# Kernel tuning notes

Hardware: AMD Instinct MI355X
Metric: run time of the kernel (lower is better)

## Reference

```python
import math
import jax, jax.numpy as jnp
import numpy as np

B, T, DIM = 1, 2048, 2048
NH, NKV = 32, 8
HD = DIM // NH  # 64
REP = NH // NKV  # 4


def _rope(x):
    # x: [b, h, t, d]; rotates as in the torch module (half-split, concat form)
    d = x.shape[-1]
    half = d // 2
    t = x.shape[2]
    freqs = jnp.arange(half, dtype=x.dtype) / max(half, 1)
    angles = jnp.arange(t, dtype=x.dtype)[:, None] * freqs[None, :]  # [t, half]
    sin = jnp.sin(angles)[None, None]  # [1,1,t,half]
    cos = jnp.cos(angles)[None, None]
    x1, x2 = x[..., :half], x[..., half:]
    return jnp.concatenate([x1 * cos - x2 * sin, x1 * sin + x2 * cos], axis=-1)


def setup_inputs() -> dict:
    key = jax.random.key(0)
    k1, k2, k3 = jax.random.split(key, 3)
    sd = 1.0 / math.sqrt(DIM)
    return {
        "x": jax.random.normal(k1, (B, T, DIM), dtype=jnp.float32),
        "Wqkv": jax.random.normal(k2, ((NH + 2 * NKV) * HD, DIM), dtype=jnp.float32) * sd,
        "Wproj": jax.random.normal(k3, (DIM, DIM), dtype=jnp.float32) * sd,
        "q_gain": jnp.ones((NH,), dtype=jnp.float32),
        "attn_temp": jnp.ones((NH,), dtype=jnp.float32),
    }


def reference(x, Wqkv, Wproj, q_gain, attn_temp):
    b, t, c = x.shape
    qkv = x @ Wqkv.T  # [b, t, (NH+2*NKV)*HD]
    q, k, v = jnp.split(qkv, [NH * HD, (NH + NKV) * HD], axis=2)
    q = q.reshape(b, t, NH, HD).transpose(0, 2, 1, 3)   # [b, NH, t, HD]
    k = k.reshape(b, t, NKV, HD).transpose(0, 2, 1, 3)  # [b, NKV, t, HD]
    v = v.reshape(b, t, NKV, HD).transpose(0, 2, 1, 3)
    # GQA expand (repeat_interleave along head axis)
    k = jnp.repeat(k, REP, axis=1)  # [b, NH, t, HD]
    v = jnp.repeat(v, REP, axis=1)
    q = _rope(q)
    k = _rope(k)
    q = q * (q_gain * attn_temp)[None, :, None, None]
    scale = 1.0 / math.sqrt(HD)
    scores = jnp.einsum('bhqd,bhkd->bhqk', q, k) * scale
    causal = jnp.tril(jnp.ones((t, t), dtype=bool))
    scores = jnp.where(causal[None, None], scores, jnp.finfo(scores.dtype).min)
    attn = jax.nn.softmax(scores, axis=-1)
    y = jnp.einsum('bhqk,bhkd->bhqd', attn, v)  # [b, NH, t, HD]
    y = y.transpose(0, 2, 1, 3).reshape(b, t, c)
    return y @ Wproj.T
```

## Files before the change

### kernel.cpp

```cpp
#include <hip/hip_runtime.h>
#include <hip/hip_bf16.h>
#include <math.h>

typedef unsigned short u16;
typedef __attribute__((ext_vector_type(8))) short short8;
typedef __attribute__((ext_vector_type(4))) float f32x4;
typedef __attribute__((ext_vector_type(4))) unsigned short u16x4;
typedef __attribute__((ext_vector_type(4))) unsigned int u32x4;

#define DEVI static __device__ __forceinline__

DEVI u16 f2bf(float f){
  union { float f; unsigned u; } c; c.f = f;
  unsigned r = (c.u + 0x7fffu + ((c.u >> 16) & 1u)) >> 16;
  return (u16)r;
}

DEVI unsigned cvtpk(float lo, float hi){
  unsigned r;
  asm("v_cvt_pk_bf16_f32 %0, %1, %2" : "=v"(r) : "v"(lo), "v"(hi));
  return r;
}

DEVI void async16(const void* g, void* l){
  __builtin_amdgcn_global_load_lds(
    (const __attribute__((address_space(1))) unsigned int*)g,
    (__attribute__((address_space(3))) unsigned int*)l, 16, 0, 0);
}

#define WAIT_BAR(N) asm volatile("s_waitcnt vmcnt(" #N ") lgkmcnt(0)\n\ts_barrier" ::: "memory")

#define ACHUNK(r, g) (((r) << 2) | (((g) + ((r) >> 1)) & 3))
#define KCH(r, g) (((r) << 3) | (((g) + (r)) & 7))

__global__ __launch_bounds__(256) void cvt3(const float4* __restrict__ x,
                                            const float4* __restrict__ wq,
                                            const float4* __restrict__ wp,
                                            u16* __restrict__ xb,
                                            u16* __restrict__ wqb,
                                            u16* __restrict__ wpb){
  int i = blockIdx.x * 256 + threadIdx.x;
  const float4* s; u16* d; int off;
  if (i < 1048576)      { s = x;  d = xb;  off = i; }
  else if (i < 2621440) { s = wq; d = wqb; off = i - 1048576; }
  else                  { s = wp; d = wpb; off = i - 2621440; }
  float4 v = s[off];
  u16x4 o;
  o.x = f2bf(v.x); o.y = f2bf(v.y); o.z = f2bf(v.z); o.w = f2bf(v.w);
  *(u16x4*)(d + (size_t)off * 4) = o;
}

__global__ __launch_bounds__(256) void gemm_qkv(const u16* __restrict__ A,
                                                const u16* __restrict__ B,
                                                const float* __restrict__ qg,
                                                const float* __restrict__ at_,
                                                u16* __restrict__ qb,
                                                u16* __restrict__ kb,
                                                u16* __restrict__ vT){
  const int K = 2048;
  __shared__ __align__(16) u16 As[4][4096];
  __shared__ __align__(16) u16 Bs[4][4096];
  const int bid = blockIdx.x;
  const int xcd = bid & 7, pos = bid >> 3;
  const int xm = xcd & 1, xn = xcd >> 1;
  const int mIdx = xm * 8 + (pos & 7);
  const int nIdx = xn * 6 + (pos >> 3);
  const int tid  = threadIdx.x;
  const int lane = tid & 63, wid = tid >> 6;
  const int wr = wid >> 1, wc = wid & 1;
  const int fr = lane & 15, fg = lane >> 4;
  const int mBase = mIdx * 128, nBase = nIdx * 128;

  f32x4 acc[4][4];
  for (int m = 0; m < 4; ++m)
    for (int n = 0; n < 4; ++n)
      for (int e = 0; e < 4; ++e) acc[m][n][e] = 0.f;

  const int c0 = tid, c1 = tid + 256;
  const int p0 = c0 >> 2, q0 = ((c0 & 3) - (p0 >> 1)) & 3;
  const int p1 = c1 >> 2, q1 = ((c1 & 3) - (p1 >> 1)) & 3;
  const u16* Ab = A + (size_t)mBase * K;
  const u16* Bb = B + (size_t)nBase * K;

  int ca[4], cb[4];
#pragma unroll
  for (int m = 0; m < 4; ++m){ const int r = wr * 64 + m * 16 + fr; ca[m] = ACHUNK(r, fg); }
#pragma unroll
  for (int n = 0; n < 4; ++n){ const int r = wc * 64 + n * 16 + fr; cb[n] = ACHUNK(r, fg); }

#define STAGE_QKV(kt) do {                                                 \
    const int b_ = (kt) & 3;                                               \
    const int kO_ = (kt) * 32;                                             \
    async16(Ab + (size_t)p0 * K + kO_ + q0 * 8, As[b_] + c0 * 8);          \
    async16(Ab + (size_t)p1 * K + kO_ + q1 * 8, As[b_] + c1 * 8);          \
    async16(Bb + (size_t)p0 * K + kO_ + q0 * 8, Bs[b_] + c0 * 8);          \
    async16(Bb + (size_t)p1 * K + kO_ + q1 * 8, Bs[b_] + c1 * 8);          \
  } while (0)

  STAGE_QKV(0); STAGE_QKV(1); STAGE_QKV(2); STAGE_QKV(3);

#pragma unroll 1
  for (int p = 0; p < 32; ++p){
    if (p < 31) WAIT_BAR(8);
    else        WAIT_BAR(0);
#pragma unroll
    for (int kk = 0; kk < 2; ++kk){
      const int cur = (2 * p + kk) & 3;
      short8 a[4], b[4];
#pragma unroll
      for (int m = 0; m < 4; ++m)
        a[m] = *(const short8*)(As[cur] + ca[m] * 8);
#pragma unroll
      for (int n = 0; n < 4; ++n)
        b[n] = *(const short8*)(Bs[cur] + cb[n] * 8);
      __builtin_amdgcn_s_setprio(1);
#pragma unroll
      for (int m = 0; m < 4; ++m)
#pragma unroll
        for (int n = 0; n < 4; ++n)
          acc[m][n] = __builtin_amdgcn_mfma_f32_16x16x32_bf16(a[m], b[n], acc[m][n], 0, 0, 0);
      __builtin_amdgcn_s_setprio(0);
    }
    __builtin_amdgcn_s_barrier();
    if (p < 30){ STAGE_QKV(2 * p + 4); STAGE_QKV(2 * p + 5); }
  }
#undef STAGE_QKV

  const int nb64 = nIdx * 2 + wc;
  if (nb64 < 40){
    const bool isq = nb64 < 32;
    const int h = isq ? nb64 : (nb64 - 32);
    const float gsc = isq ? (qg[h] * at_[h] * 0.125f) : 1.0f;
    u16* dst = isq ? qb : kb;
#pragma unroll
    for (int m = 0; m < 4; ++m)
#pragma unroll
      for (int e = 0; e < 4; ++e){
        const int t = mBase + wr * 64 + m * 16 + fg * 4 + e;
        const float ft = (float)t;
#pragma unroll
        for (int np = 0; np < 2; ++np){
          const int d = np * 16 + fr;
          const float ang = ft * ((float)d * 0.03125f);
          float sn, cs; sincosf(ang, &sn, &cs);
          const float x1 = acc[m][np][e], x2 = acc[m][np + 2][e];
          u16* base = dst + ((size_t)h * 2048 + t) * 64 + d;
          base[0]  = f2bf((x1 * cs - x2 * sn) * gsc);
          base[32] = f2bf((x1 * sn + x2 * cs) * gsc);
        }
      }
  } else {
    const int h = nb64 - 40;
#pragma unroll
    for (int m = 0; m < 4; ++m){
      const int t0 = mBase + wr * 64 + m * 16 + fg * 4;
#pragma unroll
      for (int n = 0; n < 4; ++n){
        const int d = n * 16 + fr;
        u16x4 pk;
#pragma unroll
        for (int e = 0; e < 4; ++e) pk[e] = f2bf(acc[m][n][e]);
        *(u16x4*)(vT + ((size_t)h * 64 + d) * 2048 + t0) = pk;
      }
    }
  }
}

__global__ __launch_bounds__(256) void attn_fwd(const u16* __restrict__ qb,
                                                const u16* __restrict__ kb,
                                                const u16* __restrict__ vT,
                                                u16* __restrict__ yb){
  const int bx = blockIdx.x, h = blockIdx.y;
  const int hk = h >> 2;
  const int tid = threadIdx.x;
  const int lane = tid & 63, wid = tid >> 6;
  const int fr = lane & 15, fg = lane >> 4;

  __shared__ __align__(16) u16 Ks[2][4096];
  __shared__ __align__(16) u16 Vs[2][4096];

  const u16* kbh = kb + (size_t)hk * 2048 * 64;
  const u16* vTh = vT + (size_t)hk * 64 * 2048;

  const int c0 = tid, c1 = tid + 256;
  const int p0 = c0 >> 3, q0 = ((c0 & 7) - p0) & 7;
  const int p1 = c1 >> 3, q1 = ((c1 & 7) - p1) & 7;
  const int pr0 = ((p0 >> 5) << 5) | (((p0 >> 2) & 3) << 3) | (((p0 >> 4) & 1) << 2) | (p0 & 3);
  const int pr1 = ((p1 >> 5) << 5) | (((p1 >> 2) & 3) << 3) | (((p1 >> 4) & 1) << 2) | (p1 & 3);

  int ck[2][4];
#pragma unroll
  for (int kc = 0; kc < 2; ++kc)
#pragma unroll
    for (int cf = 0; cf < 4; ++cf)
      ck[kc][cf] = KCH(cf * 16 + fr, kc * 4 + fg);

#pragma unroll 1
  for (int seg = 0; seg < 2; ++seg){
    const int qt = seg ? (31 - bx) : bx;
    const int nt = qt + 1;
    const int qrow0 = qt * 64 + wid * 16;
    const int q = qrow0 + fr;

    short8 qf[2];
    {
      const u16* qp = qb + ((size_t)h * 2048 + q) * 64 + fg * 8;
      qf[0] = *(const short8*)(qp);
      qf[1] = *(const short8*)(qp + 32);
    }

    float mrow = -1e30f, lrow = 0.f;
    f32x4 o[4];
    for (int df = 0; df < 4; ++df)
      for (int e = 0; e < 4; ++e) o[df][e] = 0.f;

    async16(kbh + (size_t)pr0 * 64 + q0 * 8,  Ks[0] + (size_t)c0 * 8);
    async16(kbh + (size_t)pr1 * 64 + q1 * 8,  Ks[0] + (size_t)c1 * 8);
    async16(vTh + (size_t)p0 * 2048 + q0 * 8, Vs[0] + (size_t)c0 * 8);
    async16(vTh + (size_t)p1 * 2048 + q1 * 8, Vs[0] + (size_t)c1 * 8);

#pragma unroll 1
    for (int kt = 0; kt < nt; ++kt){
      const int cur = kt & 1;
      __syncthreads();
      if (kt + 1 < nt){
        const int nxt = cur ^ 1;
        const size_t kO = (size_t)(kt + 1) * 64;
        async16(kbh + (kO + pr0) * 64 + q0 * 8,        Ks[nxt] + (size_t)c0 * 8);
        async16(kbh + (kO + pr1) * 64 + q1 * 8,        Ks[nxt] + (size_t)c1 * 8);
        async16(vTh + (size_t)p0 * 2048 + kO + q0 * 8, Vs[nxt] + (size_t)c0 * 8);
        async16(vTh + (size_t)p1 * 2048 + kO + q1 * 8, Vs[nxt] + (size_t)c1 * 8);
      }
      const u16* Kb = Ks[cur];
      const u16* Vb = Vs[cur];

      f32x4 s[4];
      __builtin_amdgcn_s_setprio(1);
#pragma unroll
      for (int cf = 0; cf < 4; ++cf){
        for (int e = 0; e < 4; ++e) s[cf][e] = 0.f;
#pragma unroll
        for (int kc = 0; kc < 2; ++kc){
          short8 kf = *(const short8*)(Kb + ck[kc][cf] * 8);
          s[cf] = __builtin_amdgcn_mfma_f32_16x16x32_bf16(kf, qf[kc], s[cf], 0, 0, 0);
        }
      }
      __builtin_amdgcn_s_setprio(0);

      if (kt * 64 + 63 > qrow0){
#pragma unroll
        for (int cf = 0; cf < 4; ++cf){
          const int kb0 = kt * 64 + (cf >> 1) * 32 + (cf & 1) * 4 + fg * 8;
#pragma unroll
          for (int r = 0; r < 4; ++r)
            if (kb0 + r > q) s[cf][r] = -1e30f;
        }
      }

      float m0 = fmaxf(fmaxf(s[0][0], s[0][1]), fmaxf(s[0][2], s[0][3]));
      float m1 = fmaxf(fmaxf(s[1][0], s[1][1]), fmaxf(s[1][2], s[1][3]));
      float m2 = fmaxf(fmaxf(s[2][0], s[2][1]), fmaxf(s[2][2], s[2][3]));
      float m3 = fmaxf(fmaxf(s[3][0], s[3][1]), fmaxf(s[3][2], s[3][3]));
      float mt = fmaxf(fmaxf(m0, m1), fmaxf(m2, m3));
      mt = fmaxf(mt, __shfl_xor(mt, 16));
      mt = fmaxf(mt, __shfl_xor(mt, 32));
      if (!__all(mt <= mrow + 8.f)){
        const float mn = fmaxf(mrow, mt);
        const float al = __expf(mrow - mn);
        lrow *= al;
#pragma unroll
        for (int df = 0; df < 4; ++df)
#pragma unroll
          for (int e = 0; e < 4; ++e) o[df][e] *= al;
        mrow = mn;
      }
      float rs = 0.f;
#pragma unroll
      for (int cf = 0; cf < 4; ++cf){
#pragma unroll
        for (int r = 0; r < 4; ++r){
          s[cf][r] = __expf(s[cf][r] - mrow);
          rs += s[cf][r];
        }
      }
      rs += __shfl_xor(rs, 16);
      rs += __shfl_xor(rs, 32);
      lrow += rs;

      union { u32x4 u; short8 s8; } pb_0, pb_1;
      pb_0.u[0] = cvtpk(s[0][0], s[0][1]); pb_0.u[1] = cvtpk(s[0][2], s[0][3]);
      pb_0.u[2] = cvtpk(s[1][0], s[1][1]); pb_0.u[3] = cvtpk(s[1][2], s[1][3]);
      pb_1.u[0] = cvtpk(s[2][0], s[2][1]); pb_1.u[1] = cvtpk(s[2][2], s[2][3]);
      pb_1.u[2] = cvtpk(s[3][0], s[3][1]); pb_1.u[3] = cvtpk(s[3][2], s[3][3]);

      __builtin_amdgcn_s_setprio(1);
#pragma unroll
      for (int df = 0; df < 4; ++df){
        short8 v0 = *(const short8*)(Vb + ck[0][df] * 8);
        short8 v1 = *(const short8*)(Vb + ck[1][df] * 8);
        o[df] = __builtin_amdgcn_mfma_f32_16x16x32_bf16(v0, pb_0.s8, o[df], 0, 0, 0);
        o[df] = __builtin_amdgcn_mfma_f32_16x16x32_bf16(v1, pb_1.s8, o[df], 0, 0, 0);
      }
      __builtin_amdgcn_s_setprio(0);
    }
    __syncthreads();

    const float inv = 1.f / lrow;
#pragma unroll
    for (int df = 0; df < 4; ++df){
      u16x4 pk;
#pragma unroll
      for (int e = 0; e < 4; ++e) pk[e] = f2bf(o[df][e] * inv);
      *(u16x4*)(yb + (size_t)q * 2048 + h * 64 + df * 16 + fg * 4) = pk;
    }
  }
}

__global__ __launch_bounds__(256) void gemm_bt(const u16* __restrict__ A,
                                               const u16* __restrict__ B,
                                               float* __restrict__ C,
                                               int M, int N, int K){
  __shared__ __align__(16) u16 As[4][4096];
  __shared__ __align__(16) u16 Bs[4][4096];
  const int bid = blockIdx.x;
  const int xcd = bid & 7, pos = bid >> 3;
  const int xm = xcd & 1, xn = xcd >> 1;
  const int mIdx = xm * 8 + (pos & 7);
  const int nIdx = xn * 4 + (pos >> 3);
  const int tid  = threadIdx.x;
  const int lane = tid & 63, wid = tid >> 6;
  const int wr = wid >> 1, wc = wid & 1;
  const int fr = lane & 15, fg = lane >> 4;
  const int mBase = mIdx * 128, nBase = nIdx * 128;

  f32x4 acc[4][4];
  for (int m = 0; m < 4; ++m)
    for (int n = 0; n < 4; ++n)
      for (int e = 0; e < 4; ++e) acc[m][n][e] = 0.f;

  const int c0 = tid, c1 = tid + 256;
  const int p0 = c0 >> 2, q0 = ((c0 & 3) - (p0 >> 1)) & 3;
  const int p1 = c1 >> 2, q1 = ((c1 & 3) - (p1 >> 1)) & 3;
  const u16* Ab = A + (size_t)mBase * K;
  const u16* Bb = B + (size_t)nBase * K;

  int ca[4], cb[4];
#pragma unroll
  for (int m = 0; m < 4; ++m){ const int r = wr * 64 + m * 16 + fr; ca[m] = ACHUNK(r, fg); }
#pragma unroll
  for (int n = 0; n < 4; ++n){ const int r = wc * 64 + n * 16 + fr; cb[n] = ACHUNK(r, fg); }

#define STAGE_BT(kt) do {                                                  \
    const int b_ = (kt) & 3;                                               \
    const int kO_ = (kt) * 32;                                             \
    async16(Ab + (size_t)p0 * K + kO_ + q0 * 8, As[b_] + c0 * 8);          \
    async16(Ab + (size_t)p1 * K + kO_ + q1 * 8, As[b_] + c1 * 8);          \
    async16(Bb + (size_t)p0 * K + kO_ + q0 * 8, Bs[b_] + c0 * 8);          \
    async16(Bb + (size_t)p1 * K + kO_ + q1 * 8, Bs[b_] + c1 * 8);          \
  } while (0)

  STAGE_BT(0); STAGE_BT(1); STAGE_BT(2); STAGE_BT(3);

  const int np = K >> 6;
#pragma unroll 1
  for (int p = 0; p < np; ++p){
    if (p < np - 1) WAIT_BAR(8);
    else            WAIT_BAR(0);
#pragma unroll
    for (int kk = 0; kk < 2; ++kk){
      const int cur = (2 * p + kk) & 3;
      short8 a[4], b[4];
#pragma unroll
      for (int m = 0; m < 4; ++m)
        a[m] = *(const short8*)(As[cur] + ca[m] * 8);
#pragma unroll
      for (int n = 0; n < 4; ++n)
        b[n] = *(const short8*)(Bs[cur] + cb[n] * 8);
      __builtin_amdgcn_s_setprio(1);
#pragma unroll
      for (int m = 0; m < 4; ++m)
#pragma unroll
        for (int n = 0; n < 4; ++n)
          acc[m][n] = __builtin_amdgcn_mfma_f32_16x16x32_bf16(a[m], b[n], acc[m][n], 0, 0, 0);
      __builtin_amdgcn_s_setprio(0);
    }
    __builtin_amdgcn_s_barrier();
    if (p < np - 2){ STAGE_BT(2 * p + 4); STAGE_BT(2 * p + 5); }
  }
#undef STAGE_BT

  for (int m = 0; m < 4; ++m){
    const int row = mBase + wr * 64 + m * 16 + fg * 4;
    for (int n = 0; n < 4; ++n){
      const int col = nBase + wc * 64 + n * 16 + fr;
      for (int e = 0; e < 4; ++e)
        C[(size_t)(row + e) * N + col] = acc[m][n][e];
    }
  }
}

extern "C" void kernel_launch(void* const* d_in, const int* in_sizes, int n_in,
                              void* d_out, int out_size, void* d_ws, size_t ws_size,
                              hipStream_t stream){
  (void)in_sizes; (void)n_in; (void)out_size; (void)ws_size;
  const float* x     = (const float*)d_in[0];
  const float* Wqkv  = (const float*)d_in[1];
  const float* Wproj = (const float*)d_in[2];
  const float* qg    = (const float*)d_in[3];
  const float* at    = (const float*)d_in[4];
  float* out = (float*)d_out;

  u16* xb     = (u16*)d_ws;
  u16* wqkvb  = xb + 4194304;
  u16* wprojb = wqkvb + 6291456;
  u16* qbuf   = wprojb + 4194304;
  u16* kbuf   = qbuf + 4194304;
  u16* vTb    = kbuf + 1048576;
  u16* ybuf   = vTb + 1048576;

  cvt3<<<14336, 256, 0, stream>>>((const float4*)x, (const float4*)Wqkv,
                                  (const float4*)Wproj, xb, wqkvb, wprojb);
  gemm_qkv<<<384, 256, 0, stream>>>(xb, wqkvb, qg, at, qbuf, kbuf, vTb);
  attn_fwd<<<dim3(16, 32), 256, 0, stream>>>(qbuf, kbuf, vTb, ybuf);
  gemm_bt<<<256, 256, 0, stream>>>(ybuf, wprojb, out, 2048, 2048, 2048);
}
```

Baseline: 136.1 us.

## Deepen attention K/V prefetch to a four-buffer three-ahead pipeline

Replaces the double-buffered K/V shared-memory staging in the attention kernel with four buffers and prefetches three tiles ahead, using counted async waits plus a barrier so loads stay in flight across iterations. The goal is to hide global-load latency behind the MFMA work. In exchange, LDS use per block doubles to 64KB, which may lower occupancy, and correctness depends on the WAIT_BAR counts matching the outstanding async loads.

```diff
diff --git a/kernel.cpp b/kernel.cpp
--- a/kernel.cpp
+++ b/kernel.cpp
@@ -176,8 +176,8 @@
   const int lane = tid & 63, wid = tid >> 6;
   const int fr = lane & 15, fg = lane >> 4;
 
-  __shared__ __align__(16) u16 Ks[2][4096];
-  __shared__ __align__(16) u16 Vs[2][4096];
+  __shared__ __align__(16) u16 Ks[4][4096];
+  __shared__ __align__(16) u16 Vs[4][4096];
 
   const u16* kbh = kb + (size_t)hk * 2048 * 64;
   const u16* vTh = vT + (size_t)hk * 64 * 2048;
@@ -194,6 +194,15 @@
 #pragma unroll
     for (int cf = 0; cf < 4; ++cf)
       ck[kc][cf] = KCH(cf * 16 + fr, kc * 4 + fg);
+
+#define STAGE_KV(kt) do {                                                   \
+    const int b_ = (kt) & 3;                                                \
+    const size_t kO_ = (size_t)(kt) * 64;                                   \
+    async16(kbh + (kO_ + pr0) * 64 + q0 * 8,        Ks[b_] + (size_t)c0 * 8); \
+    async16(kbh + (kO_ + pr1) * 64 + q1 * 8,        Ks[b_] + (size_t)c1 * 8); \
+    async16(vTh + (size_t)p0 * 2048 + kO_ + q0 * 8, Vs[b_] + (size_t)c0 * 8); \
+    async16(vTh + (size_t)p1 * 2048 + kO_ + q1 * 8, Vs[b_] + (size_t)c1 * 8); \
+  } while (0)
 
 #pragma unroll 1
   for (int seg = 0; seg < 2; ++seg){
@@ -214,25 +223,18 @@
     for (int df = 0; df < 4; ++df)
       for (int e = 0; e < 4; ++e) o[df][e] = 0.f;
 
-    async16(kbh + (size_t)pr0 * 64 + q0 * 8,  Ks[0] + (size_t)c0 * 8);
-    async16(kbh + (size_t)pr1 * 64 + q1 * 8,  Ks[0] + (size_t)c1 * 8);
-    async16(vTh + (size_t)p0 * 2048 + q0 * 8, Vs[0] + (size_t)c0 * 8);
-    async16(vTh + (size_t)p1 * 2048 + q1 * 8, Vs[0] + (size_t)c1 * 8);
+    STAGE_KV(0);
+    if (nt > 1) STAGE_KV(1);
+    if (nt > 2) STAGE_KV(2);
 
 #pragma unroll 1
     for (int kt = 0; kt < nt; ++kt){
-      const int cur = kt & 1;
-      __syncthreads();
-      if (kt + 1 < nt){
-        const int nxt = cur ^ 1;
-        const size_t kO = (size_t)(kt + 1) * 64;
-        async16(kbh + (kO + pr0) * 64 + q0 * 8,        Ks[nxt] + (size_t)c0 * 8);
-        async16(kbh + (kO + pr1) * 64 + q1 * 8,        Ks[nxt] + (size_t)c1 * 8);
-        async16(vTh + (size_t)p0 * 2048 + kO + q0 * 8, Vs[nxt] + (size_t)c0 * 8);
-        async16(vTh + (size_t)p1 * 2048 + kO + q1 * 8, Vs[nxt] + (size_t)c1 * 8);
-      }
-      const u16* Kb = Ks[cur];
-      const u16* Vb = Vs[cur];
+      const int rem = nt - 1 - kt;
+      if (rem >= 2)      WAIT_BAR(8);
+      else if (rem == 1) WAIT_BAR(4);
+      else               WAIT_BAR(0);
+      const u16* Kb = Ks[kt & 3];
+      const u16* Vb = Vs[kt & 3];
 
       f32x4 s[4];
       __builtin_amdgcn_s_setprio(1);
@@ -302,8 +304,10 @@
         o[df] = __builtin_amdgcn_mfma_f32_16x16x32_bf16(v1, pb_1.s8, o[df], 0, 0, 0);
       }
       __builtin_amdgcn_s_setprio(0);
-    }
-    __syncthreads();
+
+      __builtin_amdgcn_s_barrier();
+      if (kt + 3 < nt) STAGE_KV(kt + 3);
+    }
 
     const float inv = 1.f / lrow;
 #pragma unroll
@@ -314,6 +318,7 @@
       *(u16x4*)(yb + (size_t)q * 2048 + h * 64 + df * 16 + fg * 4) = pk;
     }
   }
+#undef STAGE_KV
 }
 
 __global__ __launch_bounds__(256) void gemm_bt(const u16* __restrict__ A,
```

After: 134.3 us. About the same (-1.3%).

## Use 128-key tiles in attention and fold log2e into Q for exp2

Applied to the files above, without the earlier changes.

The attention kernel now processes 128 keys per iteration instead of 64, so there are half as many loop iterations, barriers and softmax reductions, and each LDS tile is larger. This needs a new swizzle for the V tile and doubles shared memory per block. The Q scale now includes log2(e) so the softmax can call exp2f directly, and the lazy-rescale threshold is adjusted to match. The trade-off is more shared memory and registers, which may lower occupancy, plus more wasted masked work on diagonal tiles.

```diff
diff --git a/kernel.cpp b/kernel.cpp
--- a/kernel.cpp
+++ b/kernel.cpp
@@ -32,6 +32,7 @@
 
 #define ACHUNK(r, g) (((r) << 2) | (((g) + ((r) >> 1)) & 3))
 #define KCH(r, g) (((r) << 3) | (((g) + (r)) & 7))
+#define VCH(d, g) (((d) << 4) | (((g) + (d)) & 15))
 
 __global__ __launch_bounds__(256) void cvt3(const float4* __restrict__ x,
                                             const float4* __restrict__ wq,
@@ -130,7 +131,7 @@
   if (nb64 < 40){
     const bool isq = nb64 < 32;
     const int h = isq ? nb64 : (nb64 - 32);
-    const float gsc = isq ? (qg[h] * at_[h] * 0.125f) : 1.0f;
+    const float gsc = isq ? (qg[h] * at_[h] * 0.125f * 1.44269504f) : 1.0f;
     u16* dst = isq ? qb : kb;
 #pragma unroll
     for (int m = 0; m < 4; ++m)
@@ -176,29 +177,48 @@
   const int lane = tid & 63, wid = tid >> 6;
   const int fr = lane & 15, fg = lane >> 4;
 
-  __shared__ __align__(16) u16 Ks[2][4096];
-  __shared__ __align__(16) u16 Vs[2][4096];
+  __shared__ __align__(16) u16 Ks[2][8192];
+  __shared__ __align__(16) u16 Vs[2][8192];
 
   const u16* kbh = kb + (size_t)hk * 2048 * 64;
   const u16* vTh = vT + (size_t)hk * 64 * 2048;
 
-  const int c0 = tid, c1 = tid + 256;
-  const int p0 = c0 >> 3, q0 = ((c0 & 7) - p0) & 7;
-  const int p1 = c1 >> 3, q1 = ((c1 & 7) - p1) & 7;
-  const int pr0 = ((p0 >> 5) << 5) | (((p0 >> 2) & 3) << 3) | (((p0 >> 4) & 1) << 2) | (p0 & 3);
-  const int pr1 = ((p1 >> 5) << 5) | (((p1 >> 2) & 3) << 3) | (((p1 >> 4) & 1) << 2) | (p1 & 3);
-
-  int ck[2][4];
-#pragma unroll
-  for (int kc = 0; kc < 2; ++kc)
-#pragma unroll
-    for (int cf = 0; cf < 4; ++cf)
-      ck[kc][cf] = KCH(cf * 16 + fr, kc * 4 + fg);
+  int kq_[4], kpr[4], vd_[4], vg_[4];
+#pragma unroll
+  for (int j = 0; j < 4; ++j){
+    const int c = tid + j * 256;
+    const int kp = c >> 3;  kq_[j] = ((c & 7) - kp) & 7;
+    kpr[j] = ((kp >> 5) << 5) | (((kp >> 2) & 3) << 3) | (((kp >> 4) & 1) << 2) | (kp & 3);
+    vd_[j] = c >> 4;        vg_[j] = ((c & 15) - vd_[j]) & 15;
+  }
+
+  int ck[2][8], cv[4][4];
+#pragma unroll
+  for (int kcd = 0; kcd < 2; ++kcd)
+#pragma unroll
+    for (int cf = 0; cf < 8; ++cf)
+      ck[kcd][cf] = KCH(cf * 16 + fr, kcd * 4 + fg);
+#pragma unroll
+  for (int kc = 0; kc < 4; ++kc)
+#pragma unroll
+    for (int df = 0; df < 4; ++df)
+      cv[kc][df] = VCH(df * 16 + fr, kc * 4 + fg);
+
+#define STAGE_KV(kt, b) do {                                                  \
+    const size_t kO_ = (size_t)(kt) * 128;                                    \
+    _Pragma("unroll")                                                         \
+    for (int j = 0; j < 4; ++j){                                              \
+      const int c_ = tid + j * 256;                                           \
+      async16(kbh + (kO_ + kpr[j]) * 64 + kq_[j] * 8, Ks[b] + (size_t)c_ * 8);\
+      async16(vTh + (size_t)vd_[j] * 2048 + kO_ + vg_[j] * 8,                 \
+              Vs[b] + (size_t)c_ * 8);                                        \
+    }                                                                         \
+  } while (0)
 
 #pragma unroll 1
   for (int seg = 0; seg < 2; ++seg){
     const int qt = seg ? (31 - bx) : bx;
-    const int nt = qt + 1;
+    const int nt = (qt + 2) >> 1;
     const int qrow0 = qt * 64 + wid * 16;
     const int q = qrow0 + fr;
 
@@ -214,59 +234,48 @@
     for (int df = 0; df < 4; ++df)
       for (int e = 0; e < 4; ++e) o[df][e] = 0.f;
 
-    async16(kbh + (size_t)pr0 * 64 + q0 * 8,  Ks[0] + (size_t)c0 * 8);
-    async16(kbh + (size_t)pr1 * 64 + q1 * 8,  Ks[0] + (size_t)c1 * 8);
-    async16(vTh + (size_t)p0 * 2048 + q0 * 8, Vs[0] + (size_t)c0 * 8);
-    async16(vTh + (size_t)p1 * 2048 + q1 * 8, Vs[0] + (size_t)c1 * 8);
+    STAGE_KV(0, 0);
 
 #pragma unroll 1
     for (int kt = 0; kt < nt; ++kt){
       const int cur = kt & 1;
       __syncthreads();
-      if (kt + 1 < nt){
-        const int nxt = cur ^ 1;
-        const size_t kO = (size_t)(kt + 1) * 64;
-        async16(kbh + (kO + pr0) * 64 + q0 * 8,        Ks[nxt] + (size_t)c0 * 8);
-        async16(kbh + (kO + pr1) * 64 + q1 * 8,        Ks[nxt] + (size_t)c1 * 8);
-        async16(vTh + (size_t)p0 * 2048 + kO + q0 * 8, Vs[nxt] + (size_t)c0 * 8);
-        async16(vTh + (size_t)p1 * 2048 + kO + q1 * 8, Vs[nxt] + (size_t)c1 * 8);
-      }
+      if (kt + 1 < nt) STAGE_KV(kt + 1, cur ^ 1);
       const u16* Kb = Ks[cur];
       const u16* Vb = Vs[cur];
 
-      f32x4 s[4];
+      f32x4 s[8];
       __builtin_amdgcn_s_setprio(1);
 #pragma unroll
-      for (int cf = 0; cf < 4; ++cf){
+      for (int cf = 0; cf < 8; ++cf){
         for (int e = 0; e < 4; ++e) s[cf][e] = 0.f;
 #pragma unroll
-        for (int kc = 0; kc < 2; ++kc){
-          short8 kf = *(const short8*)(Kb + ck[kc][cf] * 8);
-          s[cf] = __builtin_amdgcn_mfma_f32_16x16x32_bf16(kf, qf[kc], s[cf], 0, 0, 0);
+        for (int kcd = 0; kcd < 2; ++kcd){
+          short8 kf = *(const short8*)(Kb + ck[kcd][cf] * 8);
+          s[cf] = __builtin_amdgcn_mfma_f32_16x16x32_bf16(kf, qf[kcd], s[cf], 0, 0, 0);
         }
       }
       __builtin_amdgcn_s_setprio(0);
 
-      if (kt * 64 + 63 > qrow0){
-#pragma unroll
-        for (int cf = 0; cf < 4; ++cf){
-          const int kb0 = kt * 64 + (cf >> 1) * 32 + (cf & 1) * 4 + fg * 8;
+      if (kt * 128 + 127 > qrow0){
+#pragma unroll
+        for (int cf = 0; cf < 8; ++cf){
+          const int kb0 = kt * 128 + (cf >> 1) * 32 + (cf & 1) * 4 + fg * 8;
 #pragma unroll
           for (int r = 0; r < 4; ++r)
             if (kb0 + r > q) s[cf][r] = -1e30f;
         }
       }
 
-      float m0 = fmaxf(fmaxf(s[0][0], s[0][1]), fmaxf(s[0][2], s[0][3]));
-      float m1 = fmaxf(fmaxf(s[1][0], s[1][1]), fmaxf(s[1][2], s[1][3]));
-      float m2 = fmaxf(fmaxf(s[2][0], s[2][1]), fmaxf(s[2][2], s[2][3]));
-      float m3 = fmaxf(fmaxf(s[3][0], s[3][1]), fmaxf(s[3][2], s[3][3]));
-      float mt = fmaxf(fmaxf(m0, m1), fmaxf(m2, m3));
+      float mt = -1e30f;
+#pragma unroll
+      for (int cf = 0; cf < 8; ++cf)
+        mt = fmaxf(mt, fmaxf(fmaxf(s[cf][0], s[cf][1]), fmaxf(s[cf][2], s[cf][3])));
       mt = fmaxf(mt, __shfl_xor(mt, 16));
       mt = fmaxf(mt, __shfl_xor(mt, 32));
-      if (!__all(mt <= mrow + 8.f)){
+      if (!__all(mt <= mrow + 11.5416f)){
         const float mn = fmaxf(mrow, mt);
-        const float al = __expf(mrow - mn);
+        const float al = exp2f(mrow - mn);
         lrow *= al;
 #pragma unroll
         for (int df = 0; df < 4; ++df)
@@ -276,10 +285,10 @@
       }
       float rs = 0.f;
 #pragma unroll
-      for (int cf = 0; cf < 4; ++cf){
+      for (int cf = 0; cf < 8; ++cf){
 #pragma unroll
         for (int r = 0; r < 4; ++r){
-          s[cf][r] = __expf(s[cf][r] - mrow);
+          s[cf][r] = exp2f(s[cf][r] - mrow);
           rs += s[cf][r];
         }
       }
@@ -287,19 +296,23 @@
       rs += __shfl_xor(rs, 32);
       lrow += rs;
 
-      union { u32x4 u; short8 s8; } pb_0, pb_1;
-      pb_0.u[0] = cvtpk(s[0][0], s[0][1]); pb_0.u[1] = cvtpk(s[0][2], s[0][3]);
-      pb_0.u[2] = cvtpk(s[1][0], s[1][1]); pb_0.u[3] = cvtpk(s[1][2], s[1][3]);
-      pb_1.u[0] = cvtpk(s[2][0], s[2][1]); pb_1.u[1] = cvtpk(s[2][2], s[2][3]);
-      pb_1.u[2] = cvtpk(s[3][0], s[3][1]); pb_1.u[3] = cvtpk(s[3][2], s[3][3]);
+      union { u32x4 u; short8 s8; } pb[4];
+#pragma unroll
+      for (int kc = 0; kc < 4; ++kc){
+        pb[kc].u[0] = cvtpk(s[kc * 2][0],     s[kc * 2][1]);
+        pb[kc].u[1] = cvtpk(s[kc * 2][2],     s[kc * 2][3]);
+        pb[kc].u[2] = cvtpk(s[kc * 2 + 1][0], s[kc * 2 + 1][1]);
+        pb[kc].u[3] = cvtpk(s[kc * 2 + 1][2], s[kc * 2 + 1][3]);
+      }
 
       __builtin_amdgcn_s_setprio(1);
 #pragma unroll
       for (int df = 0; df < 4; ++df){
-        short8 v0 = *(const short8*)(Vb + ck[0][df] * 8);
-        short8 v1 = *(const short8*)(Vb + ck[1][df] * 8);
-        o[df] = __builtin_amdgcn_mfma_f32_16x16x32_bf16(v0, pb_0.s8, o[df], 0, 0, 0);
-        o[df] = __builtin_amdgcn_mfma_f32_16x16x32_bf16(v1, pb_1.s8, o[df], 0, 0, 0);
+#pragma unroll
+        for (int kc = 0; kc < 4; ++kc){
+          short8 v = *(const short8*)(Vb + cv[kc][df] * 8);
+          o[df] = __builtin_amdgcn_mfma_f32_16x16x32_bf16(v, pb[kc].s8, o[df], 0, 0, 0);
+        }
       }
       __builtin_amdgcn_s_setprio(0);
     }
@@ -314,6 +327,7 @@
       *(u16x4*)(yb + (size_t)q * 2048 + h * 64 + df * 16 + fg * 4) = pk;
     }
   }
+#undef STAGE_KV
 }
 
 __global__ __launch_bounds__(256) void gemm_bt(const u16* __restrict__ A,
```

Result: slower. 140.0 us (+2.9%).
